# Kernel tuning notes

Hardware: AMD Instinct MI355X
Metric: run time of the kernel (lower is better)

## Reference

```python
import jax, jax.numpy as jnp
import numpy as np

N_NEURONS, RANK, N_CONV, LY, LX, BATCH = 8192, 1, 64, 36, 36, 256


def setup_inputs() -> dict:
    key = jax.random.key(0)
    k1, k2, k3, k4 = jax.random.split(key, 4)
    conv = jax.random.normal(k1, (BATCH, N_CONV, LY, LX), dtype=jnp.float32)
    Wc = 0.01 * jax.random.normal(k2, (N_NEURONS, RANK, N_CONV), dtype=jnp.float32)
    Wy = 0.01 * jax.random.normal(k3, (N_NEURONS, RANK, LY), dtype=jnp.float32)
    Wx = 0.01 * jax.random.normal(k4, (N_NEURONS, RANK, LX), dtype=jnp.float32)
    bias = jnp.zeros((N_NEURONS,), dtype=jnp.float32)
    return {"conv": conv, "Wc": Wc, "Wy": Wy, "Wx": Wx, "bias": bias}


def reference(conv, Wc, Wy, Wx, bias):
    # yx_separable, rank == 1 path of Readout.forward:
    #   pred = einsum('nrc,nry,icyx,nrx->in', Wc, Wy, conv, Wx)
    #   pred = elu(pred + bias)
    # Staged contraction: build per-neuron rank-1 spatial filter, contract
    # spatial dims first (small y*x=1296), then channels.
    Wyx = jnp.einsum('nry,nrx->nryx', Wy, Wx)              # [N, R, Ly, Lx]
    s = jnp.einsum('icyx,nryx->inrc', conv, Wyx)           # [B, N, R, C]
    pred = jnp.einsum('inrc,nrc->in', s, Wc)               # [B, N]
    return jax.nn.elu(pred + bias)
```

## Files before the change

kernel.cpp:

```cpp
#include <hip/hip_runtime.h>
#include <hip/hip_bf16.h>

#define NNEUR 8192
#define NCONV 64
#define LYC   36
#define LXC   36
#define BATCH 256
#define KRAW  1296
#define KPAD  1344
#define KITER 21
#define MROWS 16384
#define BM 256
#define BN 256
#define BK 64
#define CH_PER_IT 2048
#define TILE_H (KITER * CH_PER_IT * 8)
#define A_NTILES 64
#define B_NTILES 32
#define A_PREP_BLOCKS 10752
#define B_PREP_BLOCKS 5376

typedef __attribute__((ext_vector_type(8))) _Float16 half8;
typedef __attribute__((ext_vector_type(4))) float f32x4;
typedef __attribute__((ext_vector_type(16))) float f32x16;

__device__ __forceinline__ void async_copy16(const void* g, void* l) {
  __builtin_amdgcn_global_load_lds(
      (const __attribute__((address_space(1))) void*)g,
      (__attribute__((address_space(3))) void*)l, 16, 0, 0);
}

__global__ __launch_bounds__(256) void prep_kernel(
    const float* __restrict__ conv, const float* __restrict__ Wy,
    const float* __restrict__ Wx, _Float16* __restrict__ A,
    _Float16* __restrict__ B) {
  const int t = threadIdx.x;
  half8 h;
  if (blockIdx.x < A_PREP_BLOCKS) {
    const int gid = blockIdx.x * 256 + t;
    const int tile = gid / (KITER * CH_PER_IT);
    const int rem = gid - tile * (KITER * CH_PER_IT);
    const int it = rem >> 11, idx = rem & 2047;
    const int r = idx >> 3, slot = idx & 7;
    const int c = (slot - r) & 7;
    const int k0 = it * 64 + c * 8;
    const int grow = tile * BM + r;
    if (k0 < KRAW) {
      const float* s = conv + (size_t)grow * KRAW + k0;
#pragma unroll
      for (int e = 0; e < 8; e++) h[e] = (_Float16)s[e];
    } else {
#pragma unroll
      for (int e = 0; e < 8; e++) h[e] = (_Float16)0.f;
    }
    *(half8*)(A + (size_t)tile * TILE_H + (size_t)rem * 8) = h;
  } else {
    const int gid = (blockIdx.x - A_PREP_BLOCKS) * 256 + t;
    const int tile = gid / (KITER * CH_PER_IT);
    const int rem = gid - tile * (KITER * CH_PER_IT);
    const int it = rem >> 11, idx = rem & 2047;
    const int r = idx >> 3, slot = idx & 7;
    const int c = (slot - r) & 7;
    const int k0 = it * 64 + c * 8;
    const int n = tile * BN + r;
#pragma unroll
    for (int e = 0; e < 8; e++) {
      const int k = k0 + e;
      float v = 0.f;
      if (k < KRAW) {
        const int y = k / LXC;
        const int x = k - y * LXC;
        v = Wy[n * LYC + y] * Wx[n * LXC + x] * 256.f;
      }
      h[e] = (_Float16)v;
    }
    *(half8*)(B + (size_t)tile * TILE_H + (size_t)rem * 8) = h;
  }
}

__global__ __launch_bounds__(512, 2) void gemm_fused_kernel(
    const _Float16* __restrict__ A, const _Float16* __restrict__ B,
    const float* __restrict__ Wc, const float* __restrict__ bias,
    float* __restrict__ out) {
  __shared__ _Float16 As[BM * BK];
  __shared__ _Float16 Bs[BN * BK];

  const int bid = blockIdx.x;
  const int l = bid >> 3;
  const int ntile = (bid & 7) * 4 + (l & 3);
  const int mtile = l >> 2;

  const int t = threadIdx.x;
  const int lane = t & 63;
  const int wave = t >> 6;
  const int wm = wave >> 2, wn = wave & 3;
  const int r32 = lane & 31, hh = lane >> 5;

  f32x16 acc[4][2] = {};

  const _Float16* sA = A + (size_t)mtile * TILE_H + t * 8;
  const _Float16* sB = B + (size_t)ntile * TILE_H + t * 8;
  _Float16* lA = As + t * 8;
  _Float16* lB = Bs + t * 8;

  for (int it = 0; it < KITER; it++) {
#pragma unroll
    for (int i = 0; i < 4; i++) async_copy16(sA + i * 4096, lA + i * 4096);
#pragma unroll
    for (int i = 0; i < 4; i++) async_copy16(sB + i * 4096, lB + i * 4096);
    sA += CH_PER_IT * 8;
    sB += CH_PER_IT * 8;
    __syncthreads();

#pragma unroll
    for (int ks = 0; ks < 4; ks++) {
      const int cc = 2 * ks + hh;
      half8 bf[2];
#pragma unroll
      for (int nb = 0; nb < 2; nb++) {
        const int r = wn * 64 + nb * 32 + r32;
        bf[nb] = *(const half8*)(Bs + r * 64 + ((cc + r) & 7) * 8);
      }
#pragma unroll
      for (int mb = 0; mb < 4; mb++) {
        const int r = wm * 128 + mb * 32 + r32;
        const half8 af = *(const half8*)(As + r * 64 + ((cc + r) & 7) * 8);
#pragma unroll
        for (int nb = 0; nb < 2; nb++)
          acc[mb][nb] = __builtin_amdgcn_mfma_f32_32x32x16_f16(
              af, bf[nb], acc[mb][nb], 0, 0, 0);
      }
    }
    __syncthreads();
  }

  const int ibase = mtile * 4 + wm * 2;
  float v[2][2];
#pragma unroll
  for (int nb = 0; nb < 2; nb++) {
    const int n_g = ntile * BN + wn * 64 + nb * 32 + r32;
    const float* wc = Wc + (size_t)n_g * NCONV;
    f32x4 w[2][4];
#pragma unroll
    for (int hf = 0; hf < 2; hf++)
#pragma unroll
      for (int g = 0; g < 4; g++)
        w[hf][g] = *(const f32x4*)(wc + hf * 32 + hh * 4 + g * 8);
#pragma unroll
    for (int img = 0; img < 2; img++) {
      float p = 0.f;
#pragma unroll
      for (int hf = 0; hf < 2; hf++)
#pragma unroll
        for (int g = 0; g < 4; g++)
#pragma unroll
          for (int q = 0; q < 4; q++)
            p += acc[img * 2 + hf][nb][g * 4 + q] * w[hf][g][q];
      p += __shfl_xor(p, 32);
      v[img][nb] = p;
    }
  }
  const int img = ibase + hh;
#pragma unroll
  for (int nb = 0; nb < 2; nb++) {
    const int n_out = ntile * BN + wn * 64 + nb * 32 + r32;
    float z = v[hh][nb] * 0.00390625f + bias[n_out];
    z = z > 0.f ? z : (__expf(z) - 1.f);
    out[(size_t)img * NNEUR + n_out] = z;
  }
}

extern "C" void kernel_launch(void* const* d_in, const int* in_sizes, int n_in,
                              void* d_out, int out_size, void* d_ws,
                              size_t ws_size, hipStream_t stream) {
  const float* conv = (const float*)d_in[0];
  const float* Wc = (const float*)d_in[1];
  const float* Wy = (const float*)d_in[2];
  const float* Wx = (const float*)d_in[3];
  const float* bias = (const float*)d_in[4];
  float* out = (float*)d_out;

  _Float16* Abuf = (_Float16*)d_ws;
  _Float16* Bbuf =
      (_Float16*)((char*)d_ws + (size_t)A_NTILES * TILE_H * 2);

  prep_kernel<<<A_PREP_BLOCKS + B_PREP_BLOCKS, 256, 0, stream>>>(conv, Wy, Wx,
                                                                 Abuf, Bbuf);
  gemm_fused_kernel<<<2048, 512, 0, stream>>>(Abuf, Bbuf, Wc, bias, out);
}
```

Before: 514.0 us.

## Double-buffer LDS with BK=32 k-major layout and 4-wave 128x128 warp tiles

```diff
diff --git a/kernel.cpp b/kernel.cpp
--- a/kernel.cpp
+++ b/kernel.cpp
@@ -7,18 +7,17 @@
 #define LXC   36
 #define BATCH 256
 #define KRAW  1296
-#define KPAD  1344
-#define KITER 21
+#define KITER 42
+#define BK    32
 #define MROWS 16384
 #define BM 256
 #define BN 256
-#define BK 64
-#define CH_PER_IT 2048
-#define TILE_H (KITER * CH_PER_IT * 8)
+#define CH_IT 1024
+#define TILE_H (KITER * CH_IT * 8)
 #define A_NTILES 64
 #define B_NTILES 32
-#define A_PREP_BLOCKS 10752
-#define B_PREP_BLOCKS 5376
+#define A_PREP_BLOCKS (A_NTILES * KITER)
+#define B_PREP_BLOCKS (B_NTILES * KITER)
 
 typedef __attribute__((ext_vector_type(8))) _Float16 half8;
 typedef __attribute__((ext_vector_type(4))) float f32x4;
@@ -35,55 +34,67 @@
     const float* __restrict__ Wx, _Float16* __restrict__ A,
     _Float16* __restrict__ B) {
   const int t = threadIdx.x;
-  half8 h;
   if (blockIdx.x < A_PREP_BLOCKS) {
-    const int gid = blockIdx.x * 256 + t;
-    const int tile = gid / (KITER * CH_PER_IT);
-    const int rem = gid - tile * (KITER * CH_PER_IT);
-    const int it = rem >> 11, idx = rem & 2047;
-    const int r = idx >> 3, slot = idx & 7;
-    const int c = (slot - r) & 7;
-    const int k0 = it * 64 + c * 8;
-    const int grow = tile * BM + r;
-    if (k0 < KRAW) {
-      const float* s = conv + (size_t)grow * KRAW + k0;
-#pragma unroll
-      for (int e = 0; e < 8; e++) h[e] = (_Float16)s[e];
-    } else {
-#pragma unroll
-      for (int e = 0; e < 8; e++) h[e] = (_Float16)0.f;
-    }
-    *(half8*)(A + (size_t)tile * TILE_H + (size_t)rem * 8) = h;
+    const int tile = blockIdx.x / KITER;
+    const int it = blockIdx.x - tile * KITER;
+    __shared__ _Float16 sm[256 * 40];
+#pragma unroll
+    for (int i = 0; i < 8; i++) {
+      const int idx = i * 256 + t;
+      const int r = idx >> 3, j = idx & 7;
+      const int k0 = it * BK + j * 4;
+      float4 f = make_float4(0.f, 0.f, 0.f, 0.f);
+      if (k0 + 3 < KRAW)
+        f = *(const float4*)(conv + (size_t)(tile * BM + r) * KRAW + k0);
+      _Float16* d = sm + r * 40 + j * 4;
+      d[0] = (_Float16)f.x; d[1] = (_Float16)f.y;
+      d[2] = (_Float16)f.z; d[3] = (_Float16)f.w;
+    }
+    __syncthreads();
+#pragma unroll
+    for (int i = 0; i < 4; i++) {
+      const int idx = i * 256 + t;
+      const int c = idx >> 8, r = idx & 255;
+      const _Float16* s = sm + r * 40 + c * 8;
+      half8 h;
+#pragma unroll
+      for (int e = 0; e < 8; e++) h[e] = s[e];
+      *(half8*)(A + (size_t)tile * TILE_H + (size_t)it * (CH_IT * 8) +
+                (size_t)idx * 8) = h;
+    }
   } else {
-    const int gid = (blockIdx.x - A_PREP_BLOCKS) * 256 + t;
-    const int tile = gid / (KITER * CH_PER_IT);
-    const int rem = gid - tile * (KITER * CH_PER_IT);
-    const int it = rem >> 11, idx = rem & 2047;
-    const int r = idx >> 3, slot = idx & 7;
-    const int c = (slot - r) & 7;
-    const int k0 = it * 64 + c * 8;
-    const int n = tile * BN + r;
-#pragma unroll
-    for (int e = 0; e < 8; e++) {
-      const int k = k0 + e;
-      float v = 0.f;
-      if (k < KRAW) {
-        const int y = k / LXC;
-        const int x = k - y * LXC;
-        v = Wy[n * LYC + y] * Wx[n * LXC + x] * 256.f;
+    const int b = blockIdx.x - A_PREP_BLOCKS;
+    const int tile = b / KITER;
+    const int it = b - tile * KITER;
+#pragma unroll
+    for (int i = 0; i < 4; i++) {
+      const int idx = i * 256 + t;
+      const int c = idx >> 8, r = idx & 255;
+      const int n = tile * BN + r;
+      const int k0 = it * BK + c * 8;
+      half8 h;
+#pragma unroll
+      for (int e = 0; e < 8; e++) {
+        const int k = k0 + e;
+        float v = 0.f;
+        if (k < KRAW) {
+          const int y = k / LXC;
+          const int x = k - y * LXC;
+          v = Wy[n * LYC + y] * Wx[n * LXC + x] * 256.f;
+        }
+        h[e] = (_Float16)v;
       }
-      h[e] = (_Float16)v;
-    }
-    *(half8*)(B + (size_t)tile * TILE_H + (size_t)rem * 8) = h;
-  }
-}
-
-__global__ __launch_bounds__(512, 2) void gemm_fused_kernel(
+      *(half8*)(B + (size_t)tile * TILE_H + (size_t)it * (CH_IT * 8) +
+                (size_t)idx * 8) = h;
+    }
+  }
+}
+
+__global__ __launch_bounds__(256, 1) void gemm_fused_kernel(
     const _Float16* __restrict__ A, const _Float16* __restrict__ B,
     const float* __restrict__ Wc, const float* __restrict__ bias,
     float* __restrict__ out) {
-  __shared__ _Float16 As[BM * BK];
-  __shared__ _Float16 Bs[BN * BK];
+  __shared__ _Float16 lds[2][(BM + BN) * BK];
 
   const int bid = blockIdx.x;
   const int l = bid >> 3;
@@ -93,52 +104,61 @@
   const int t = threadIdx.x;
   const int lane = t & 63;
   const int wave = t >> 6;
-  const int wm = wave >> 2, wn = wave & 3;
+  const int wm = wave >> 1, wn = wave & 1;
   const int r32 = lane & 31, hh = lane >> 5;
 
-  f32x16 acc[4][2] = {};
-
-  const _Float16* sA = A + (size_t)mtile * TILE_H + t * 8;
-  const _Float16* sB = B + (size_t)ntile * TILE_H + t * 8;
-  _Float16* lA = As + t * 8;
-  _Float16* lB = Bs + t * 8;
-
-  for (int it = 0; it < KITER; it++) {
-#pragma unroll
-    for (int i = 0; i < 4; i++) async_copy16(sA + i * 4096, lA + i * 4096);
-#pragma unroll
-    for (int i = 0; i < 4; i++) async_copy16(sB + i * 4096, lB + i * 4096);
-    sA += CH_PER_IT * 8;
-    sB += CH_PER_IT * 8;
+  f32x16 acc[4][4] = {};
+
+  const _Float16* pA = A + (size_t)mtile * TILE_H + t * 8;
+  const _Float16* pB = B + (size_t)ntile * TILE_H + t * 8;
+
+#pragma unroll
+  for (int i = 0; i < 4; i++)
+    async_copy16(pA + i * 2048, &lds[0][0] + t * 8 + i * 2048);
+#pragma unroll
+  for (int i = 0; i < 4; i++)
+    async_copy16(pB + i * 2048, &lds[0][BM * BK] + t * 8 + i * 2048);
+
+  int cur = 0;
+  for (int it = 0; it < KITER; ++it) {
     __syncthreads();
-
-#pragma unroll
-    for (int ks = 0; ks < 4; ks++) {
+    if (it + 1 < KITER) {
+      const _Float16* nA = pA + (size_t)(it + 1) * (CH_IT * 8);
+      const _Float16* nB = pB + (size_t)(it + 1) * (CH_IT * 8);
+      _Float16* dA = &lds[cur ^ 1][0] + t * 8;
+      _Float16* dB = &lds[cur ^ 1][BM * BK] + t * 8;
+#pragma unroll
+      for (int i = 0; i < 4; i++) async_copy16(nA + i * 2048, dA + i * 2048);
+#pragma unroll
+      for (int i = 0; i < 4; i++) async_copy16(nB + i * 2048, dB + i * 2048);
+    }
+    const _Float16* As_ = &lds[cur][0];
+    const _Float16* Bs_ = &lds[cur][BM * BK];
+#pragma unroll
+    for (int ks = 0; ks < 2; ++ks) {
       const int cc = 2 * ks + hh;
-      half8 bf[2];
-#pragma unroll
-      for (int nb = 0; nb < 2; nb++) {
-        const int r = wn * 64 + nb * 32 + r32;
-        bf[nb] = *(const half8*)(Bs + r * 64 + ((cc + r) & 7) * 8);
-      }
-#pragma unroll
-      for (int mb = 0; mb < 4; mb++) {
-        const int r = wm * 128 + mb * 32 + r32;
-        const half8 af = *(const half8*)(As + r * 64 + ((cc + r) & 7) * 8);
-#pragma unroll
-        for (int nb = 0; nb < 2; nb++)
+      half8 af[4], bf[4];
+#pragma unroll
+      for (int mb = 0; mb < 4; mb++)
+        af[mb] = *(const half8*)(As_ + cc * 2048 + (wm * 128 + mb * 32 + r32) * 8);
+#pragma unroll
+      for (int nb = 0; nb < 4; nb++)
+        bf[nb] = *(const half8*)(Bs_ + cc * 2048 + (wn * 128 + nb * 32 + r32) * 8);
+#pragma unroll
+      for (int mb = 0; mb < 4; mb++)
+#pragma unroll
+        for (int nb = 0; nb < 4; nb++)
           acc[mb][nb] = __builtin_amdgcn_mfma_f32_32x32x16_f16(
-              af, bf[nb], acc[mb][nb], 0, 0, 0);
-      }
-    }
-    __syncthreads();
+              af[mb], bf[nb], acc[mb][nb], 0, 0, 0);
+    }
+    cur ^= 1;
   }
 
   const int ibase = mtile * 4 + wm * 2;
-  float v[2][2];
-#pragma unroll
-  for (int nb = 0; nb < 2; nb++) {
-    const int n_g = ntile * BN + wn * 64 + nb * 32 + r32;
+  float v[2][4];
+#pragma unroll
+  for (int nb = 0; nb < 4; nb++) {
+    const int n_g = ntile * BN + wn * 128 + nb * 32 + r32;
     const float* wc = Wc + (size_t)n_g * NCONV;
     f32x4 w[2][4];
 #pragma unroll
@@ -162,8 +182,8 @@
   }
   const int img = ibase + hh;
 #pragma unroll
-  for (int nb = 0; nb < 2; nb++) {
-    const int n_out = ntile * BN + wn * 64 + nb * 32 + r32;
+  for (int nb = 0; nb < 4; nb++) {
+    const int n_out = ntile * BN + wn * 128 + nb * 32 + r32;
     float z = v[hh][nb] * 0.00390625f + bias[n_out];
     z = z > 0.f ? z : (__expf(z) - 1.f);
     out[(size_t)img * NNEUR + n_out] = z;
@@ -186,5 +206,5 @@
 
   prep_kernel<<<A_PREP_BLOCKS + B_PREP_BLOCKS, 256, 0, stream>>>(conv, Wy, Wx,
                                                                  Abuf, Bbuf);
-  gemm_fused_kernel<<<2048, 512, 0, stream>>>(Abuf, Bbuf, Wc, bias, out);
-}
+  gemm_fused_kernel<<<2048, 256, 0, stream>>>(Abuf, Bbuf, Wc, bias, out);
+}
```

Result: slower. 553.5 us (+7.7%).
